# Kernel tuning notes

Measured on AMD Instinct MI355X. Metric: run time of the kernel, lower is better.

## Reference

```python
import jax, jax.numpy as jnp
import numpy as np

D_MODEL = 1024
NUM_HEADS = 16
D_K = D_MODEL // NUM_HEADS


def setup_inputs() -> dict:
    key = jax.random.key(0)
    ks = jax.random.split(key, 11)
    s = 1.0 / np.sqrt(D_MODEL)
    return {
        "Q": jax.random.normal(ks[0], (2, 2048, D_MODEL), jnp.float32),
        "K": jax.random.normal(ks[1], (2, 2048, D_MODEL), jnp.float32),
        "V": jax.random.normal(ks[2], (2, 2048, D_MODEL), jnp.float32),
        "W_Q": jax.random.uniform(ks[3], (D_MODEL, D_MODEL), jnp.float32, -s, s),
        "b_Q": jax.random.uniform(ks[4], (D_MODEL,), jnp.float32, -s, s),
        "W_K": jax.random.uniform(ks[5], (D_K, D_MODEL), jnp.float32, -s, s),
        "b_K": jax.random.uniform(ks[6], (D_K,), jnp.float32, -s, s),
        "W_V": jax.random.uniform(ks[7], (D_K, D_MODEL), jnp.float32, -s, s),
        "b_V": jax.random.uniform(ks[8], (D_K,), jnp.float32, -s, s),
        "W_O": jax.random.uniform(ks[9], (D_MODEL, D_MODEL), jnp.float32, -s, s),
        "b_O": jax.random.uniform(ks[10], (D_MODEL,), jnp.float32, -s, s),
    }


def reference(Q, K, V, W_Q, b_Q, W_K, b_K, W_V, b_V, W_O, b_O):
    B, S, _ = Q.shape
    # Q projection -> [B, H, S, d_k]
    q = (Q @ W_Q.T + b_Q).reshape(B, S, NUM_HEADS, D_K).transpose(0, 2, 1, 3)
    # shared single-head K/V -> [B, S, d_k] (broadcast across heads)
    k = K @ W_K.T + b_K
    v = V @ W_V.T + b_V
    scale = 1.0 / jnp.sqrt(jnp.asarray(D_K, q.dtype))
    scores = jnp.einsum('bhqd,bkd->bhqk', q, k) * scale  # [B,H,S,S]
    attn = jax.nn.softmax(scores, axis=-1)
    out = jnp.einsum('bhqk,bkd->bhqd', attn, v)  # [B,H,S,d_k]
    out = out.transpose(0, 2, 1, 3).reshape(B, S, D_MODEL)
    return out @ W_O.T + b_O
```

## Files before the change

kernel.cpp:

```cpp
#include <hip/hip_runtime.h>
#include <hip/hip_bf16.h>
#include <math.h>

#define D_MODEL 1024
#define NUM_HEADS 16
#define DK 64
#define BATCH 2
#define SEQ 2048
#define MROWS (BATCH * SEQ)

#define QSCALE (0.125f * 1.4426950408889634f)

typedef __attribute__((ext_vector_type(8))) short bf16x8;
typedef __attribute__((ext_vector_type(4))) float f32x4;

static __device__ __forceinline__ short f2bf(float f) {
    __hip_bfloat16 h = __float2bfloat16(f);
    union { __hip_bfloat16 h; short s; } c; c.h = h; return c.s;
}

static __device__ __forceinline__ unsigned pkbf2(float a, float b) {
    __hip_bfloat162 h = __float22bfloat162_rn(make_float2(a, b));
    union { __hip_bfloat162 h; unsigned u; } c; c.h = h; return c.u;
}

static __device__ __forceinline__ void gload16(const void* g, void* l) {
    __builtin_amdgcn_global_load_lds(
        (const __attribute__((address_space(1))) unsigned int*)g,
        (__attribute__((address_space(3))) unsigned int*)l, 16, 0, 0);
}

__global__ __launch_bounds__(256) void cvt6(
    const float* __restrict__ q, const float* __restrict__ k,
    const float* __restrict__ v, const float* __restrict__ wq,
    const float* __restrict__ wo, const float* __restrict__ wk,
    const float* __restrict__ wv,
    short* __restrict__ qo, short* __restrict__ ko, short* __restrict__ vo,
    short* __restrict__ wqo, short* __restrict__ woo, short* __restrict__ wko,
    short* __restrict__ wvo)
{
    const int NB = (MROWS * D_MODEL) / 8;
    const int NW = (D_MODEL * D_MODEL) / 8;
    const int NS = (DK * D_MODEL) / 8;
    const int total = 3 * NB + 2 * NW + 2 * NS;
    for (int g = blockIdx.x * 256 + threadIdx.x; g < total; g += gridDim.x * 256) {
        const float* s; short* d; int x = g;
        if (x < NB)            { s = q;  d = qo;  }
        else if ((x -= NB) < NB) { s = k;  d = ko;  }
        else if ((x -= NB) < NB) { s = v;  d = vo;  }
        else if ((x -= NB) < NW) { s = wq; d = wqo; }
        else if ((x -= NW) < NW) { s = wo; d = woo; }
        else if ((x -= NW) < NS) { s = wk; d = wko; }
        else                     { x -= NS; s = wv; d = wvo; }
        float4 a = ((const float4*)s)[x * 2];
        float4 b = ((const float4*)s)[x * 2 + 1];
        uint4 hv;
        hv.x = pkbf2(a.x, a.y); hv.y = pkbf2(a.z, a.w);
        hv.z = pkbf2(b.x, b.y); hv.w = pkbf2(b.z, b.w);
        ((uint4*)d)[x] = hv;
    }
}

template<int MODE, int BM, int BN>
__global__ __launch_bounds__(256) void gemm97(
    const short* __restrict__ A, const short* __restrict__ W,
    const float* __restrict__ bias, void* __restrict__ Cp,
    const short* __restrict__ A2, const short* __restrict__ W2,
    const float* __restrict__ bias2, void* __restrict__ Cp2,
    int M, int N, int K, float outmult)
{
    constexpr int MI = BM / 32;
    constexpr int NI = BN / 32;
    constexpr int ACH = BM / 32;
    constexpr int WCH = BN / 32;
    __shared__ short As[2][BM * 64];
    __shared__ short Ws[2][BN * 64];

    int sel = 0;
    if (MODE == 2) {
        sel = blockIdx.y;
        if (sel) { A = A2; W = W2; bias = bias2; Cp = Cp2; }
    }
    const int bm = blockIdx.x * BM;
    const int bn = (MODE == 2) ? 0 : blockIdx.y * BN;
    const int tid = threadIdx.x;
    const int l = tid & 63, w = tid >> 6;
    const int lr = l & 15, lg = l >> 4;
    const int wm = (w >> 1) * (BM / 2), wn = (w & 1) * (BN / 2);

    f32x4 acc[MI][NI];
    #pragma unroll
    for (int mi = 0; mi < MI; mi++)
        #pragma unroll
        for (int ni = 0; ni < NI; ni++)
            acc[mi][ni] = (f32x4){0.f, 0.f, 0.f, 0.f};

    const int srow = l >> 3;
    const int scol = (l & 7) * 8;

    auto stage = [&](int t, int buf) {
        const int k0 = t * 64;
        #pragma unroll
        for (int i = 0; i < ACH; i++) {
            int c = w * ACH + i;
            gload16(A + (size_t)(bm + 8 * c + srow) * K + k0 + scol, &As[buf][c * 512]);
        }
        #pragma unroll
        for (int i = 0; i < WCH; i++) {
            int c = w * WCH + i;
            gload16(W + (size_t)(bn + 8 * c + srow) * K + k0 + scol, &Ws[buf][c * 512]);
        }
    };

    const int NT = K / 64;
    stage(0, 0);

    for (int t = 0; t < NT; t++) {
        const int cur = t & 1;
        __syncthreads();
        if (t + 1 < NT) stage(t + 1, cur ^ 1);
        #pragma unroll
        for (int ks = 0; ks < 2; ks++) {
            bf16x8 af[MI], bf[NI];
            #pragma unroll
            for (int mi = 0; mi < MI; mi++)
                af[mi] = *(const bf16x8*)&As[cur][(wm + mi * 16 + lr) * 64 + ks * 32 + 8 * lg];
            #pragma unroll
            for (int ni = 0; ni < NI; ni++)
                bf[ni] = *(const bf16x8*)&Ws[cur][(wn + ni * 16 + lr) * 64 + ks * 32 + 8 * lg];
            #pragma unroll
            for (int mi = 0; mi < MI; mi++)
                #pragma unroll
                for (int ni = 0; ni < NI; ni++)
                    acc[mi][ni] = __builtin_amdgcn_mfma_f32_16x16x32_bf16(
                        af[mi], bf[ni], acc[mi][ni], 0, 0, 0);
        }
    }

    #pragma unroll
    for (int ni = 0; ni < NI; ni++) {
        int col = bn + wn + ni * 16 + lr;
        float bv = bias[col];
        #pragma unroll
        for (int mi = 0; mi < MI; mi++) {
            #pragma unroll
            for (int r = 0; r < 4; r++) {
                int row = bm + wm + mi * 16 + lg * 4 + r;
                float val = (acc[mi][ni][r] + bv) * outmult;
                if (MODE == 0) {
                    ((short*)Cp)[(size_t)row * N + col] = f2bf(val);
                } else if (MODE == 1) {
                    ((float*)Cp)[(size_t)row * N + col] = val;
                } else {
                    if (sel == 0) {
                        ((short*)Cp)[(size_t)row * DK + col] = f2bf(val);
                    } else {
                        int bi = row >> 11, si = row & (SEQ - 1);
                        int s6 = si & 63;
                        int sperm = (si & ~63) | (s6 & 32) |
                                    (((s6 >> 3) & 1) << 4) | (((s6 >> 2) & 1) << 3) |
                                    (((s6 >> 4) & 1) << 2) | (s6 & 3);
                        ((short*)Cp)[((size_t)bi * DK + col) * SEQ + sperm] = f2bf(val);
                    }
                }
            }
        }
    }
}

__global__ __launch_bounds__(256, 4) void mqa_attn_lds(
    const short* __restrict__ qb, const short* __restrict__ kb,
    const short* __restrict__ vt, short* __restrict__ ob)
{
    __shared__ char KsB[2][64 * 128];
    __shared__ char VsB[2][64 * 128];
    const int h = blockIdx.y, b = blockIdx.z;
    const int tid = threadIdx.x;
    const int l = tid & 63, w = tid >> 6;
    const int lr = l & 15, lg = l >> 4;
    const int q0 = blockIdx.x * 64 + w * 16;

    bf16x8 qf[2];
    #pragma unroll
    for (int kk = 0; kk < 2; kk++)
        qf[kk] = *(const bf16x8*)(
            qb + (size_t)(b * SEQ + q0 + lr) * D_MODEL + h * DK + kk * 32 + 8 * lg);

    int srow[2], scol[2];
    #pragma unroll
    for (int i = 0; i < 2; i++) {
        int s = i * 256 + w * 64 + l;
        srow[i] = s >> 3;
        int cb = (s & 7) * 16;
        scol[i] = (cb ^ ((srow[i] & 7) << 4)) >> 1;
    }

    f32x4 o[4];
    #pragma unroll
    for (int dt = 0; dt < 4; dt++)
        o[dt] = (f32x4){0.f, 0.f, 0.f, 0.f};
    float m_i = -1e30f;
    float l_l = 0.f;

    #pragma unroll
    for (int i = 0; i < 2; i++) {
        gload16(kb + (size_t)(b * SEQ + 0 + srow[i]) * DK + scol[i],
                KsB[0] + (i * 256 + w * 64) * 16);
        gload16(vt + (size_t)(b * DK + srow[i]) * SEQ + 0 + scol[i],
                VsB[0] + (i * 256 + w * 64) * 16);
    }

    for (int t = 0; t < SEQ / 64; t++) {
        const int cur = t & 1;
        const int kt = t * 64;
        __syncthreads();
        if (t + 1 < SEQ / 64) {
            const int ktn = kt + 64;
            #pragma unroll
            for (int i = 0; i < 2; i++) {
                gload16(kb + (size_t)(b * SEQ + ktn + srow[i]) * DK + scol[i],
                        KsB[cur ^ 1] + (i * 256 + w * 64) * 16);
                gload16(vt + (size_t)(b * DK + srow[i]) * SEQ + ktn + scol[i],
                        VsB[cur ^ 1] + (i * 256 + w * 64) * 16);
            }
        }
        const char* Kc = KsB[cur];
        const char* Vc = VsB[cur];

        f32x4 s[4];
        #pragma unroll
        for (int j = 0; j < 4; j++) s[j] = (f32x4){0.f, 0.f, 0.f, 0.f};
        #pragma unroll
        for (int kk = 0; kk < 2; kk++) {
            bf16x8 kf[4];
            #pragma unroll
            for (int j = 0; j < 4; j++) {
                int row = j * 16 + lr;
                kf[j] = *(const bf16x8*)(Kc + row * 128 + ((kk * 64 + 16 * lg) ^ ((row & 7) << 4)));
            }
            __builtin_amdgcn_s_setprio(1);
            #pragma unroll
            for (int j = 0; j < 4; j++)
                s[j] = __builtin_amdgcn_mfma_f32_16x16x32_bf16(
                    kf[j], qf[kk], s[j], 0, 0, 0);
            __builtin_amdgcn_s_setprio(0);
        }

        bf16x8 vf[2][4];
        #pragma unroll
        for (int kk = 0; kk < 2; kk++)
            #pragma unroll
            for (int dt = 0; dt < 4; dt++) {
                int row = dt * 16 + lr;
                vf[kk][dt] = *(const bf16x8*)(Vc + row * 128 + ((kk * 64 + 16 * lg) ^ ((row & 7) << 4)));
            }

        union { unsigned u[4]; bf16x8 v; } pku[2];
        {
            float mA = fmaxf(fmaxf(s[0][0], s[0][1]), s[0][2]);
            float mB = fmaxf(fmaxf(s[0][3], s[1][0]), s[1][1]);
            float mC = fmaxf(fmaxf(s[1][2], s[1][3]), s[2][0]);
            float mD = fmaxf(fmaxf(s[2][1], s[2][2]), s[2][3]);
            float mE = fmaxf(fmaxf(s[3][0], s[3][1]), s[3][2]);
            float mx = fmaxf(fmaxf(fmaxf(mA, mB), mC),
                             fmaxf(fmaxf(mD, mE), s[3][3]));

            if (__any(mx > m_i + 8.0f)) {
                float mxf = fmaxf(mx, __shfl_xor(mx, 16));
                mxf = fmaxf(mxf, __shfl_xor(mxf, 32));
                float mn = fmaxf(m_i, mxf);
                float corr = __builtin_amdgcn_exp2f(m_i - mn);
                m_i = mn;
                l_l *= corr;
                #pragma unroll
                for (int dt = 0; dt < 4; dt++)
                    o[dt] *= corr;
            }
            const float mnv = m_i;

            float p[4][4];
            float rs = 0.f;
            #pragma unroll
            for (int j = 0; j < 4; j++) {
                p[j][0] = __builtin_amdgcn_exp2f(s[j][0] - mnv);
                p[j][1] = __builtin_amdgcn_exp2f(s[j][1] - mnv);
                p[j][2] = __builtin_amdgcn_exp2f(s[j][2] - mnv);
                p[j][3] = __builtin_amdgcn_exp2f(s[j][3] - mnv);
                rs += (p[j][0] + p[j][1]) + (p[j][2] + p[j][3]);
            }
            l_l += rs;

            pku[0].u[0] = pkbf2(p[0][0], p[0][1]);
            pku[0].u[1] = pkbf2(p[0][2], p[0][3]);
            pku[0].u[2] = pkbf2(p[1][0], p[1][1]);
            pku[0].u[3] = pkbf2(p[1][2], p[1][3]);
            pku[1].u[0] = pkbf2(p[2][0], p[2][1]);
            pku[1].u[1] = pkbf2(p[2][2], p[2][3]);
            pku[1].u[2] = pkbf2(p[3][0], p[3][1]);
            pku[1].u[3] = pkbf2(p[3][2], p[3][3]);
        }

        __builtin_amdgcn_s_setprio(1);
        #pragma unroll
        for (int kk = 0; kk < 2; kk++)
            #pragma unroll
            for (int dt = 0; dt < 4; dt++)
                o[dt] = __builtin_amdgcn_mfma_f32_16x16x32_bf16(
                    vf[kk][dt], pku[kk].v, o[dt], 0, 0, 0);
        __builtin_amdgcn_s_setprio(0);
    }

    float lt = l_l;
    lt += __shfl_xor(lt, 16);
    lt += __shfl_xor(lt, 32);
    float inv = 1.0f / lt;
    size_t grow = (size_t)(b * SEQ + q0 + lr);
    #pragma unroll
    for (int dt = 0; dt < 4; dt++) {
        uint2 pk;
        pk.x = pkbf2(o[dt][0] * inv, o[dt][1] * inv);
        pk.y = pkbf2(o[dt][2] * inv, o[dt][3] * inv);
        *(uint2*)(ob + grow * D_MODEL + h * DK + dt * 16 + lg * 4) = pk;
    }
}

extern "C" void kernel_launch(void* const* d_in, const int* in_sizes, int n_in,
                              void* d_out, int out_size, void* d_ws, size_t ws_size,
                              hipStream_t stream) {
    const float* Q   = (const float*)d_in[0];
    const float* K   = (const float*)d_in[1];
    const float* V   = (const float*)d_in[2];
    const float* W_Q = (const float*)d_in[3];
    const float* b_Q = (const float*)d_in[4];
    const float* W_K = (const float*)d_in[5];
    const float* b_K = (const float*)d_in[6];
    const float* W_V = (const float*)d_in[7];
    const float* b_V = (const float*)d_in[8];
    const float* W_O = (const float*)d_in[9];
    const float* b_O = (const float*)d_in[10];
    float* out = (float*)d_out;

    short* Qb  = (short*)d_ws;
    short* Kb  = Qb  + (size_t)MROWS * D_MODEL;
    short* Vb  = Kb  + (size_t)MROWS * D_MODEL;
    short* WQb = Vb  + (size_t)MROWS * D_MODEL;
    short* WKb = WQb + (size_t)D_MODEL * D_MODEL;
    short* WVb = WKb + (size_t)DK * D_MODEL;
    short* WOb = WVb + (size_t)DK * D_MODEL;
    short* qb  = WOb + (size_t)D_MODEL * D_MODEL;
    short* kb  = qb  + (size_t)MROWS * D_MODEL;
    short* vt  = kb  + (size_t)MROWS * DK;
    short* aws = vt  + (size_t)MROWS * DK;

    cvt6<<<2048, 256, 0, stream>>>(Q, K, V, W_Q, W_O, W_K, W_V,
                                   Qb, Kb, Vb, WQb, WOb, WKb, WVb);

    gemm97<0, 64, 128><<<dim3(MROWS / 64, D_MODEL / 128), 256, 0, stream>>>(
        Qb, WQb, b_Q, qb, nullptr, nullptr, nullptr, nullptr,
        MROWS, D_MODEL, D_MODEL, QSCALE);
    gemm97<2, 64, 64><<<dim3(MROWS / 64, 2), 256, 0, stream>>>(
        Kb, WKb, b_K, kb, Vb, WVb, b_V, vt, MROWS, DK, D_MODEL, 1.0f);
    mqa_attn_lds<<<dim3(SEQ / 64, NUM_HEADS, BATCH), 256, 0, stream>>>(
        qb, kb, vt, aws);
    gemm97<1, 64, 128><<<dim3(MROWS / 64, D_MODEL / 128), 256, 0, stream>>>(
        aws, WOb, b_O, out, nullptr, nullptr, nullptr, nullptr,
        MROWS, D_MODEL, D_MODEL, 1.0f);
}
```

Baseline: 127.3 us.

## Fuse fp32-to-bf16 activation conversion into projection GEMM operand loads

```diff
diff --git a/kernel.cpp b/kernel.cpp
--- a/kernel.cpp
+++ b/kernel.cpp
@@ -30,25 +30,18 @@
         (__attribute__((address_space(3))) unsigned int*)l, 16, 0, 0);
 }
 
-__global__ __launch_bounds__(256) void cvt6(
-    const float* __restrict__ q, const float* __restrict__ k,
-    const float* __restrict__ v, const float* __restrict__ wq,
-    const float* __restrict__ wo, const float* __restrict__ wk,
-    const float* __restrict__ wv,
-    short* __restrict__ qo, short* __restrict__ ko, short* __restrict__ vo,
-    short* __restrict__ wqo, short* __restrict__ woo, short* __restrict__ wko,
-    short* __restrict__ wvo)
+__global__ __launch_bounds__(256) void cvt_w(
+    const float* __restrict__ wq, const float* __restrict__ wo,
+    const float* __restrict__ wk, const float* __restrict__ wv,
+    short* __restrict__ wqo, short* __restrict__ woo,
+    short* __restrict__ wko, short* __restrict__ wvo)
 {
-    const int NB = (MROWS * D_MODEL) / 8;
     const int NW = (D_MODEL * D_MODEL) / 8;
     const int NS = (DK * D_MODEL) / 8;
-    const int total = 3 * NB + 2 * NW + 2 * NS;
+    const int total = 2 * NW + 2 * NS;
     for (int g = blockIdx.x * 256 + threadIdx.x; g < total; g += gridDim.x * 256) {
         const float* s; short* d; int x = g;
-        if (x < NB)            { s = q;  d = qo;  }
-        else if ((x -= NB) < NB) { s = k;  d = ko;  }
-        else if ((x -= NB) < NB) { s = v;  d = vo;  }
-        else if ((x -= NB) < NW) { s = wq; d = wqo; }
+        if (x < NW)              { s = wq; d = wqo; }
         else if ((x -= NW) < NW) { s = wo; d = woo; }
         else if ((x -= NW) < NS) { s = wk; d = wko; }
         else                     { x -= NS; s = wv; d = wvo; }
@@ -61,25 +54,23 @@
     }
 }
 
-template<int MODE, int BM, int BN>
+template<int MODE, int BM, int BN, int AFP32>
 __global__ __launch_bounds__(256) void gemm97(
-    const short* __restrict__ A, const short* __restrict__ W,
+    const void* __restrict__ Ap, const short* __restrict__ W,
     const float* __restrict__ bias, void* __restrict__ Cp,
-    const short* __restrict__ A2, const short* __restrict__ W2,
+    const void* __restrict__ Ap2, const short* __restrict__ W2,
     const float* __restrict__ bias2, void* __restrict__ Cp2,
     int M, int N, int K, float outmult)
 {
     constexpr int MI = BM / 32;
     constexpr int NI = BN / 32;
-    constexpr int ACH = BM / 32;
     constexpr int WCH = BN / 32;
-    __shared__ short As[2][BM * 64];
     __shared__ short Ws[2][BN * 64];
 
     int sel = 0;
     if (MODE == 2) {
         sel = blockIdx.y;
-        if (sel) { A = A2; W = W2; bias = bias2; Cp = Cp2; }
+        if (sel) { Ap = Ap2; W = W2; bias = bias2; Cp = Cp2; }
     }
     const int bm = blockIdx.x * BM;
     const int bn = (MODE == 2) ? 0 : blockIdx.y * BN;
@@ -97,43 +88,105 @@
 
     const int srow = l >> 3;
     const int scol = (l & 7) * 8;
-
-    auto stage = [&](int t, int buf) {
-        const int k0 = t * 64;
-        #pragma unroll
-        for (int i = 0; i < ACH; i++) {
-            int c = w * ACH + i;
-            gload16(A + (size_t)(bm + 8 * c + srow) * K + k0 + scol, &As[buf][c * 512]);
-        }
-        #pragma unroll
-        for (int i = 0; i < WCH; i++) {
-            int c = w * WCH + i;
-            gload16(W + (size_t)(bn + 8 * c + srow) * K + k0 + scol, &Ws[buf][c * 512]);
-        }
-    };
+    const int frow = l >> 4;
+    const int fcol = (l & 15) * 4;
 
     const int NT = K / 64;
-    stage(0, 0);
-
-    for (int t = 0; t < NT; t++) {
-        const int cur = t & 1;
-        __syncthreads();
-        if (t + 1 < NT) stage(t + 1, cur ^ 1);
-        #pragma unroll
-        for (int ks = 0; ks < 2; ks++) {
-            bf16x8 af[MI], bf[NI];
-            #pragma unroll
-            for (int mi = 0; mi < MI; mi++)
-                af[mi] = *(const bf16x8*)&As[cur][(wm + mi * 16 + lr) * 64 + ks * 32 + 8 * lg];
-            #pragma unroll
-            for (int ni = 0; ni < NI; ni++)
-                bf[ni] = *(const bf16x8*)&Ws[cur][(wn + ni * 16 + lr) * 64 + ks * 32 + 8 * lg];
-            #pragma unroll
-            for (int mi = 0; mi < MI; mi++)
+
+    if (AFP32) {
+        __shared__ float Asf[2][BM * 64];
+        const float* A = (const float*)Ap;
+        constexpr int ACHF = BM / 16;
+
+        auto stage = [&](int t, int buf) {
+            const int k0 = t * 64;
+            #pragma unroll
+            for (int i = 0; i < ACHF; i++) {
+                int c = w * ACHF + i;
+                gload16(A + (size_t)(bm + 4 * c + frow) * K + k0 + fcol,
+                        &Asf[buf][c * 256]);
+            }
+            #pragma unroll
+            for (int i = 0; i < WCH; i++) {
+                int c = w * WCH + i;
+                gload16(W + (size_t)(bn + 8 * c + srow) * K + k0 + scol,
+                        &Ws[buf][c * 512]);
+            }
+        };
+
+        stage(0, 0);
+        for (int t = 0; t < NT; t++) {
+            const int cur = t & 1;
+            __syncthreads();
+            if (t + 1 < NT) stage(t + 1, cur ^ 1);
+            #pragma unroll
+            for (int ks = 0; ks < 2; ks++) {
+                bf16x8 af[MI], bf[NI];
+                #pragma unroll
+                for (int mi = 0; mi < MI; mi++) {
+                    const float* ap = &Asf[cur][(wm + mi * 16 + lr) * 64 + ks * 32 + 8 * lg];
+                    f32x4 a0 = *(const f32x4*)ap;
+                    f32x4 a1 = *(const f32x4*)(ap + 4);
+                    union { unsigned u[4]; bf16x8 v; } ac;
+                    ac.u[0] = pkbf2(a0[0], a0[1]);
+                    ac.u[1] = pkbf2(a0[2], a0[3]);
+                    ac.u[2] = pkbf2(a1[0], a1[1]);
+                    ac.u[3] = pkbf2(a1[2], a1[3]);
+                    af[mi] = ac.v;
+                }
                 #pragma unroll
                 for (int ni = 0; ni < NI; ni++)
-                    acc[mi][ni] = __builtin_amdgcn_mfma_f32_16x16x32_bf16(
-                        af[mi], bf[ni], acc[mi][ni], 0, 0, 0);
+                    bf[ni] = *(const bf16x8*)&Ws[cur][(wn + ni * 16 + lr) * 64 + ks * 32 + 8 * lg];
+                #pragma unroll
+                for (int mi = 0; mi < MI; mi++)
+                    #pragma unroll
+                    for (int ni = 0; ni < NI; ni++)
+                        acc[mi][ni] = __builtin_amdgcn_mfma_f32_16x16x32_bf16(
+                            af[mi], bf[ni], acc[mi][ni], 0, 0, 0);
+            }
+        }
+    } else {
+        __shared__ short As[2][BM * 64];
+        const short* A = (const short*)Ap;
+        constexpr int ACH = BM / 32;
+
+        auto stage = [&](int t, int buf) {
+            const int k0 = t * 64;
+            #pragma unroll
+            for (int i = 0; i < ACH; i++) {
+                int c = w * ACH + i;
+                gload16(A + (size_t)(bm + 8 * c + srow) * K + k0 + scol,
+                        &As[buf][c * 512]);
+            }
+            #pragma unroll
+            for (int i = 0; i < WCH; i++) {
+                int c = w * WCH + i;
+                gload16(W + (size_t)(bn + 8 * c + srow) * K + k0 + scol,
+                        &Ws[buf][c * 512]);
+            }
+        };
+
+        stage(0, 0);
+        for (int t = 0; t < NT; t++) {
+            const int cur = t & 1;
+            __syncthreads();
+            if (t + 1 < NT) stage(t + 1, cur ^ 1);
+            #pragma unroll
+            for (int ks = 0; ks < 2; ks++) {
+                bf16x8 af[MI], bf[NI];
+                #pragma unroll
+                for (int mi = 0; mi < MI; mi++)
+                    af[mi] = *(const bf16x8*)&As[cur][(wm + mi * 16 + lr) * 64 + ks * 32 + 8 * lg];
+                #pragma unroll
+                for (int ni = 0; ni < NI; ni++)
+                    bf[ni] = *(const bf16x8*)&Ws[cur][(wn + ni * 16 + lr) * 64 + ks * 32 + 8 * lg];
+                #pragma unroll
+                for (int mi = 0; mi < MI; mi++)
+                    #pragma unroll
+                    for (int ni = 0; ni < NI; ni++)
+                        acc[mi][ni] = __builtin_amdgcn_mfma_f32_16x16x32_bf16(
+                            af[mi], bf[ni], acc[mi][ni], 0, 0, 0);
+            }
         }
     }
 
@@ -340,10 +393,7 @@
     const float* b_O = (const float*)d_in[10];
     float* out = (float*)d_out;
 
-    short* Qb  = (short*)d_ws;
-    short* Kb  = Qb  + (size_t)MROWS * D_MODEL;
-    short* Vb  = Kb  + (size_t)MROWS * D_MODEL;
-    short* WQb = Vb  + (size_t)MROWS * D_MODEL;
+    short* WQb = (short*)d_ws;
     short* WKb = WQb + (size_t)D_MODEL * D_MODEL;
     short* WVb = WKb + (size_t)DK * D_MODEL;
     short* WOb = WVb + (size_t)DK * D_MODEL;
@@ -352,17 +402,16 @@
     short* vt  = kb  + (size_t)MROWS * DK;
     short* aws = vt  + (size_t)MROWS * DK;
 
-    cvt6<<<2048, 256, 0, stream>>>(Q, K, V, W_Q, W_O, W_K, W_V,
-                                   Qb, Kb, Vb, WQb, WOb, WKb, WVb);
-
-    gemm97<0, 64, 128><<<dim3(MROWS / 64, D_MODEL / 128), 256, 0, stream>>>(
-        Qb, WQb, b_Q, qb, nullptr, nullptr, nullptr, nullptr,
+    cvt_w<<<512, 256, 0, stream>>>(W_Q, W_O, W_K, W_V, WQb, WOb, WKb, WVb);
+
+    gemm97<0, 64, 128, 1><<<dim3(MROWS / 64, D_MODEL / 128), 256, 0, stream>>>(
+        Q, WQb, b_Q, qb, nullptr, nullptr, nullptr, nullptr,
         MROWS, D_MODEL, D_MODEL, QSCALE);
-    gemm97<2, 64, 64><<<dim3(MROWS / 64, 2), 256, 0, stream>>>(
-        Kb, WKb, b_K, kb, Vb, WVb, b_V, vt, MROWS, DK, D_MODEL, 1.0f);
+    gemm97<2, 64, 64, 1><<<dim3(MROWS / 64, 2), 256, 0, stream>>>(
+        K, WKb, b_K, kb, V, WVb, b_V, vt, MROWS, DK, D_MODEL, 1.0f);
     mqa_attn_lds<<<dim3(SEQ / 64, NUM_HEADS, BATCH), 256, 0, stream>>>(
         qb, kb, vt, aws);
-    gemm97<1, 64, 128><<<dim3(MROWS / 64, D_MODEL / 128), 256, 0, stream>>>(
+    gemm97<1, 64, 128, 0><<<dim3(MROWS / 64, D_MODEL / 128), 256, 0, stream>>>(
         aws, WOb, b_O, out, nullptr, nullptr, nullptr, nullptr,
         MROWS, D_MODEL, D_MODEL, 1.0f);
 }
```

Measured after the change: 138.0 us. 1.08x slower.
